# Kernel optimization log

Measured on AMD Instinct MI355X. Metric: run time of the kernel, lower is better.

Reference implementation:

```python
import jax, jax.numpy as jnp
import numpy as np

B, C, N = 4, 256, 4096
C4 = C // 4  # q/k projection dim (channels // 4)
BN_EPS = 1e-5


def setup_inputs() -> dict:
    key = jax.random.key(0)
    ks = jax.random.split(key, 4)
    s = 0.05
    return {
        "x": jax.random.normal(ks[0], (B, C, N), jnp.float32),
        # q_conv and k_conv share this weight in the original module
        "wq": jax.random.normal(ks[1], (C4, C), jnp.float32) * s,
        "wv": jax.random.normal(ks[2], (C, C), jnp.float32) * s,
        "bv": jnp.zeros((C,), jnp.float32),
        "wt": jax.random.normal(ks[3], (C, C), jnp.float32) * s,
        "bt": jnp.zeros((C,), jnp.float32),
        "gamma": jnp.ones((C,), jnp.float32),
        "beta": jnp.zeros((C,), jnp.float32),
        "running_mean": jnp.zeros((C,), jnp.float32),
        "running_var": jnp.ones((C,), jnp.float32),
    }


def reference(x, wq, wv, bv, wt, bt, gamma, beta, running_mean, running_var):
    # 1x1 Conv1d == channel matmul. q/k share wq.
    q = jnp.einsum('oc,bcn->bno', wq, x)            # [B, N, C4]
    k = jnp.einsum('oc,bcn->bon', wq, x)            # [B, C4, N]
    energy = jnp.einsum('bno,bom->bnm', q, k)       # [B, N, N]
    attn = jax.nn.softmax(energy, axis=-1)
    # offset-attention L1 re-normalization over dim 1 (query axis)
    attn = attn / (1e-9 + attn.sum(axis=1, keepdims=True))
    v = jnp.einsum('oc,bcn->bon', wv, x) + bv[None, :, None]   # [B, C, N]
    # x_r[b,c,n] = sum_m v[b,c,m] * attn[b,n,m]
    x_r = jnp.einsum('bcm,bnm->bcn', v, attn)       # [B, C, N]
    t = jnp.einsum('oc,bcn->bon', wt, x - x_r) + bt[None, :, None]
    # BatchNorm1d in inference mode (running stats)
    inv = jax.lax.rsqrt(running_var + BN_EPS)
    bn = (t - running_mean[None, :, None]) * (gamma * inv)[None, :, None] + beta[None, :, None]
    return x + jax.nn.relu(bn)
```

## Files before the change

### kernel.cpp

```cpp
#include <hip/hip_runtime.h>
#include <math.h>

namespace {

constexpr int B_ = 4;
constexpr int C_ = 256;
constexpr int C4_ = 64;
constexpr int N_ = 4096;

typedef __attribute__((ext_vector_type(8))) short bf16x8;
typedef __attribute__((ext_vector_type(4))) float f32x4;

__device__ __forceinline__ unsigned short bf16_rne(float f) {
    unsigned u = __float_as_uint(f);
    u += 0x7fffu + ((u >> 16) & 1u);
    return (unsigned short)(u >> 16);
}

__device__ __forceinline__ void g2l16(const unsigned short* g, unsigned short* l) {
    __builtin_amdgcn_global_load_lds(
        (const __attribute__((address_space(1))) unsigned int*)g,
        (__attribute__((address_space(3))) unsigned int*)l, 16, 0, 0);
}

__global__ __launch_bounds__(256) void cvt_kernel(
        const float* __restrict__ wq, const float* __restrict__ wv,
        const float* __restrict__ wt, unsigned short* __restrict__ wcomb,
        unsigned short* __restrict__ wtb) {
    const int i = (blockIdx.x * 256 + threadIdx.x) * 4;
    const float* src;
    unsigned short* dst;
    if (i < 16384) { src = wq + i; dst = wcomb + i; }
    else if (i < 81920) { src = wv + (i - 16384); dst = wcomb + i; }
    else { src = wt + (i - 81920); dst = wtb + (i - 81920); }
    const float4 f = *reinterpret_cast<const float4*>(src);
    ushort4 u;
    u.x = bf16_rne(f.x); u.y = bf16_rne(f.y);
    u.z = bf16_rne(f.z); u.w = bf16_rne(f.w);
    *reinterpret_cast<ushort4*>(dst) = u;
}

__global__ __launch_bounds__(1024, 4) void proj_kernel(
        const float* __restrict__ x, const unsigned short* __restrict__ wcomb,
        const float* __restrict__ bv, unsigned short* __restrict__ qkT,
        unsigned short* __restrict__ v) {
    __shared__ unsigned short xs[2][64][40];
    const int b = blockIdx.y;
    const int n0 = blockIdx.x * 64;
    const int tid = threadIdx.x;
    const int wave = tid >> 6, lane = tid & 63;
    const int ws = wave & 3, oq = wave >> 2;
    const int quad = lane >> 4, l15 = lane & 15;
    const int ca = tid >> 6, na = tid & 63;
    const int cb = (tid + 1024) >> 6, nb2 = (tid + 1024) & 63;
    f32x4 acc[5];
#pragma unroll
    for (int ot = 0; ot < 5; ++ot) acc[ot] = (f32x4){0.f, 0.f, 0.f, 0.f};
    xs[0][na][ca] = bf16_rne(x[((size_t)b * C_ + ca) * N_ + n0 + na]);
    xs[0][nb2][cb] = bf16_rne(x[((size_t)b * C_ + cb) * N_ + n0 + nb2]);
    __syncthreads();
    for (int ch = 0; ch < 8; ++ch) {
        const int buf = ch & 1;
        float la = 0.f, lb = 0.f;
        if (ch < 7) {
            la = x[((size_t)b * C_ + (ch + 1) * 32 + ca) * N_ + n0 + na];
            lb = x[((size_t)b * C_ + (ch + 1) * 32 + cb) * N_ + n0 + nb2];
        }
        const bf16x8 a = *reinterpret_cast<const bf16x8*>(&xs[buf][ws * 16 + l15][quad * 8]);
#pragma unroll
        for (int ot = 0; ot < 5; ++ot) {
            const int gro = oq * 5 + ot;
            const bf16x8 wb = *reinterpret_cast<const bf16x8*>(
                wcomb + (size_t)(gro * 16 + l15) * C_ + ch * 32 + quad * 8);
            acc[ot] = __builtin_amdgcn_mfma_f32_16x16x32_bf16(a, wb, acc[ot], 0, 0, 0);
        }
        if (ch < 7) {
            xs[buf ^ 1][na][ca] = bf16_rne(la);
            xs[buf ^ 1][nb2][cb] = bf16_rne(lb);
        }
        __syncthreads();
    }
    const int n = n0 + ws * 16 + quad * 4;
#pragma unroll
    for (int ot = 0; ot < 5; ++ot) {
        const int gro = oq * 5 + ot;
        if (gro < 4) {
            const int o = gro * 16 + l15;
#pragma unroll
            for (int r = 0; r < 4; ++r)
                qkT[((size_t)b * N_ + n + r) * C4_ + o] = bf16_rne(acc[ot][r]);
        } else {
            const int c = (gro - 4) * 16 + l15;
            const float bb = bv[c];
            ushort4 u;
            u.x = bf16_rne(acc[ot][0] + bb);
            u.y = bf16_rne(acc[ot][1] + bb);
            u.z = bf16_rne(acc[ot][2] + bb);
            u.w = bf16_rne(acc[ot][3] + bb);
            *reinterpret_cast<ushort4*>(&v[((size_t)b * C_ + c) * N_ + n]) = u;
        }
    }
}

__global__ __launch_bounds__(1024, 4) void rowsum_kernel(
        const unsigned short* __restrict__ qkT, float* __restrict__ rowsuminv) {
    __shared__ unsigned short kt[2][64][68];
    __shared__ float red[4][4][16];
    const int b = blockIdx.y;
    const int tid = threadIdx.x;
    const int wave = tid >> 6, lane = tid & 63;
    const int ws = wave & 3, sg = wave >> 2;
    const int quad = lane >> 4, l15 = lane & 15;
    const int n0 = blockIdx.x * 64;
    const unsigned short* qb = qkT + (size_t)b * N_ * C4_;
    const unsigned short* qrow = qb + (size_t)(n0 + ws * 16 + l15) * C4_;
    const bf16x8 a0 = *reinterpret_cast<const bf16x8*>(qrow + quad * 8);
    const bf16x8 a1 = *reinterpret_cast<const bf16x8*>(qrow + 32 + quad * 8);
    const int srow = tid >> 3, soff = tid & 7;
    if (tid < 512) {
        const bf16x8 sk = *reinterpret_cast<const bf16x8*>(qb + (size_t)srow * C4_ + soff * 8);
        *reinterpret_cast<bf16x8*>(&kt[0][srow][soff * 8]) = sk;
    }
    __syncthreads();
    float cs[4] = {};
    for (int mt = 0; mt < 64; ++mt) {
        const int buf = mt & 1;
        bf16x8 nk;
        if (mt < 63 && tid < 512)
            nk = *reinterpret_cast<const bf16x8*>(
                qb + (size_t)((mt + 1) * 64 + srow) * C4_ + soff * 8);
        const bf16x8 kb0 = *reinterpret_cast<const bf16x8*>(&kt[buf][sg * 16 + l15][quad * 8]);
        const bf16x8 kb1 = *reinterpret_cast<const bf16x8*>(&kt[buf][sg * 16 + l15][32 + quad * 8]);
        f32x4 z = {0.f, 0.f, 0.f, 0.f};
        z = __builtin_amdgcn_mfma_f32_16x16x32_bf16(a0, kb0, z, 0, 0, 0);
        const f32x4 e = __builtin_amdgcn_mfma_f32_16x16x32_bf16(a1, kb1, z, 0, 0, 0);
#pragma unroll
        for (int r = 0; r < 4; ++r) cs[r] += __expf(e[r]);
        if (mt < 63 && tid < 512)
            *reinterpret_cast<bf16x8*>(&kt[buf ^ 1][srow][soff * 8]) = nk;
        __syncthreads();
    }
#pragma unroll
    for (int r = 0; r < 4; ++r) {
#pragma unroll
        for (int k = 1; k <= 8; k <<= 1) cs[r] += __shfl_xor(cs[r], k, 64);
        if (l15 == 0) red[sg][ws][quad * 4 + r] = cs[r];
    }
    __syncthreads();
    if (tid < 64) {
        const int ws2 = tid >> 4, row = tid & 15;
        const float sum = red[0][ws2][row] + red[1][ws2][row] +
                          red[2][ws2][row] + red[3][ws2][row];
        rowsuminv[(size_t)b * N_ + n0 + ws2 * 16 + row] = 1.0f / sum;
    }
}

__global__ __launch_bounds__(1024, 4) void colsum_kernel(
        const unsigned short* __restrict__ qkT, const float* __restrict__ rowsuminv,
        float* __restrict__ colsuminv) {
    __shared__ float rl[N_];
    __shared__ unsigned short qt[2][64][68];
    __shared__ float red[4][4][16];
    const int b = blockIdx.y;
    const int tid = threadIdx.x;
    const int wave = tid >> 6, lane = tid & 63;
    const int mw = wave & 3, ng = wave >> 2;
    const int quad = lane >> 4, l15 = lane & 15;
    const int m0 = blockIdx.x * 64;
    for (int i = tid; i < N_; i += 1024) rl[i] = rowsuminv[(size_t)b * N_ + i];
    const unsigned short* qb = qkT + (size_t)b * N_ * C4_;
    const unsigned short* krow = qb + (size_t)(m0 + mw * 16 + l15) * C4_;
    const bf16x8 kb0 = *reinterpret_cast<const bf16x8*>(krow + quad * 8);
    const bf16x8 kb1 = *reinterpret_cast<const bf16x8*>(krow + 32 + quad * 8);
    const int srow = tid >> 3, soff = tid & 7;
    if (tid < 512) {
        const bf16x8 sq = *reinterpret_cast<const bf16x8*>(qb + (size_t)srow * C4_ + soff * 8);
        *reinterpret_cast<bf16x8*>(&qt[0][srow][soff * 8]) = sq;
    }
    __syncthreads();
    float cs = 0.f;
    for (int nt = 0; nt < 64; ++nt) {
        const int buf = nt & 1;
        bf16x8 nq;
        if (nt < 63 && tid < 512)
            nq = *reinterpret_cast<const bf16x8*>(
                qb + (size_t)((nt + 1) * 64 + srow) * C4_ + soff * 8);
        const bf16x8 a0 = *reinterpret_cast<const bf16x8*>(&qt[buf][ng * 16 + l15][quad * 8]);
        const bf16x8 a1 = *reinterpret_cast<const bf16x8*>(&qt[buf][ng * 16 + l15][32 + quad * 8]);
        f32x4 z = {0.f, 0.f, 0.f, 0.f};
        z = __builtin_amdgcn_mfma_f32_16x16x32_bf16(a0, kb0, z, 0, 0, 0);
        const f32x4 e = __builtin_amdgcn_mfma_f32_16x16x32_bf16(a1, kb1, z, 0, 0, 0);
        const int nb = nt * 64 + ng * 16 + quad * 4;
#pragma unroll
        for (int r = 0; r < 4; ++r) cs += __expf(e[r]) * rl[nb + r];
        if (nt < 63 && tid < 512)
            *reinterpret_cast<bf16x8*>(&qt[buf ^ 1][srow][soff * 8]) = nq;
        __syncthreads();
    }
    cs += __shfl_xor(cs, 16, 64);
    cs += __shfl_xor(cs, 32, 64);
    if (quad == 0) red[ng][mw][l15] = cs;
    __syncthreads();
    if (tid < 64) {
        const int mw2 = tid >> 4, l = tid & 15;
        const float sum = red[0][mw2][l] + red[1][mw2][l] +
                          red[2][mw2][l] + red[3][mw2][l];
        colsuminv[(size_t)b * N_ + m0 + mw2 * 16 + l] = 1.0f / (1e-9f + sum);
    }
}

__global__ __launch_bounds__(1024, 4) void final_kernel(
        const float* __restrict__ x, const unsigned short* __restrict__ qkT,
        const unsigned short* __restrict__ v, const unsigned short* __restrict__ wtb,
        const float* __restrict__ rowsuminv, const float* __restrict__ colsuminv,
        const float* __restrict__ bt, const float* __restrict__ gamma,
        const float* __restrict__ beta, const float* __restrict__ rmean,
        const float* __restrict__ rvar, float* __restrict__ out) {
    __shared__ union {
        struct {
            unsigned short vt[3][256][64];
            unsigned short kt[3][64][64];
        } s;
        unsigned short dsm[64][268];
    } u;
    __shared__ unsigned short p_sh[4][16][68];
    __shared__ float ci[N_];
    const int gid = blockIdx.x;
    const int xcd = gid & 7;
    const int b = xcd >> 1;
    const int n0 = ((((unsigned)gid >> 3) << 1) | (xcd & 1)) * 64;
    const int tid = threadIdx.x;
    const int wave = tid >> 6, lane = tid & 63;
    const int ws = wave & 3, g = wave >> 2;
    const int quad = lane >> 4, l15 = lane & 15;
    const unsigned short* qb = qkT + (size_t)b * N_ * C4_;
    const unsigned short* vbg = v + (size_t)b * C_ * N_;
    const int rowA = lane >> 3;
    const int swc = ((lane & 7) ^ rowA) * 8;
    const int w8 = wave * 8;
    const int r7 = l15 & 7;
    const int c0s = (quad * 8) ^ (r7 << 3);
    const int c1s = (32 + quad * 8) ^ (r7 << 3);
    const unsigned short* qrow = qb + (size_t)(n0 + ws * 16 + l15) * C4_;
    const bf16x8 q0 = *reinterpret_cast<const bf16x8*>(qrow + quad * 8);
    const bf16x8 q1 = *reinterpret_cast<const bf16x8*>(qrow + 32 + quad * 8);
    const float rli = rowsuminv[(size_t)b * N_ + n0 + ws * 16 + l15];
    {
        const float4 c4 = *reinterpret_cast<const float4*>(colsuminv + (size_t)b * N_ + tid * 4);
        *reinterpret_cast<float4*>(&ci[tid * 4]) = c4;
    }
#define STAGE_TILE(sidx, bufS)                                                          \
    do {                                                                                \
        g2l16(vbg + (size_t)(w8 + rowA) * N_ + (sidx) * 64 + swc,                       \
              &u.s.vt[bufS][w8][0]);                                                    \
        g2l16(vbg + (size_t)(w8 + 128 + rowA) * N_ + (sidx) * 64 + swc,                 \
              &u.s.vt[bufS][w8 + 128][0]);                                              \
        if (wave < 8)                                                                   \
            g2l16(qb + (size_t)((sidx) * 64 + w8 + rowA) * C4_ + swc,                   \
                  &u.s.kt[bufS][w8][0]);                                                \
    } while (0)
    STAGE_TILE(0, 0);
    STAGE_TILE(1, 1);
    if (wave < 8) asm volatile("s_waitcnt vmcnt(3)" ::: "memory");
    else          asm volatile("s_waitcnt vmcnt(2)" ::: "memory");
    asm volatile("s_waitcnt lgkmcnt(0)" ::: "memory");
    __builtin_amdgcn_s_barrier();
    f32x4 acc[4];
#pragma unroll
    for (int j = 0; j < 4; ++j) acc[j] = (f32x4){0.f, 0.f, 0.f, 0.f};
    int bufR = 0;
#pragma unroll 1
    for (int t = 0; t < 64; ++t) {
        if (t <= 61) {
            int bufS = bufR + 2; if (bufS >= 3) bufS -= 3;
            STAGE_TILE(t + 2, bufS);
        }
        {
            const unsigned short(*ktb)[64] = u.s.kt[bufR];
            const bf16x8 ka0 = *reinterpret_cast<const bf16x8*>(&ktb[g * 16 + l15][c0s]);
            const bf16x8 ka1 = *reinterpret_cast<const bf16x8*>(&ktb[g * 16 + l15][c1s]);
            f32x4 z = {0.f, 0.f, 0.f, 0.f};
            z = __builtin_amdgcn_mfma_f32_16x16x32_bf16(ka0, q0, z, 0, 0, 0);
            z = __builtin_amdgcn_mfma_f32_16x16x32_bf16(ka1, q1, z, 0, 0, 0);
            const float4 civ = *reinterpret_cast<const float4*>(&ci[t * 64 + g * 16 + quad * 4]);
            ushort4 pk;
            pk.x = bf16_rne(__expf(z[0]) * rli * civ.x);
            pk.y = bf16_rne(__expf(z[1]) * rli * civ.y);
            pk.z = bf16_rne(__expf(z[2]) * rli * civ.z);
            pk.w = bf16_rne(__expf(z[3]) * rli * civ.w);
            *reinterpret_cast<ushort4*>(&p_sh[ws][l15][g * 16 + quad * 4]) = pk;
        }
        asm volatile("s_waitcnt lgkmcnt(0)" ::: "memory");
        __builtin_amdgcn_s_barrier();
        {
            const bf16x8 pa0 = *reinterpret_cast<const bf16x8*>(&p_sh[ws][l15][quad * 8]);
            const bf16x8 pa1 = *reinterpret_cast<const bf16x8*>(&p_sh[ws][l15][32 + quad * 8]);
            const unsigned short(*vtb)[64] = u.s.vt[bufR];
#pragma unroll
            for (int j = 0; j < 4; ++j) {
                const int vr = (g * 4 + j) * 16 + l15;
                const bf16x8 vb0 = *reinterpret_cast<const bf16x8*>(&vtb[vr][c0s]);
                const bf16x8 vb1 = *reinterpret_cast<const bf16x8*>(&vtb[vr][c1s]);
                acc[j] = __builtin_amdgcn_mfma_f32_16x16x32_bf16(pa0, vb0, acc[j], 0, 0, 0);
                acc[j] = __builtin_amdgcn_mfma_f32_16x16x32_bf16(pa1, vb1, acc[j], 0, 0, 0);
            }
        }
        asm volatile("s_waitcnt lgkmcnt(0)" ::: "memory");
        if (t <= 61) {
            if (wave < 8) asm volatile("s_waitcnt vmcnt(3)" ::: "memory");
            else          asm volatile("s_waitcnt vmcnt(2)" ::: "memory");
        } else {
            asm volatile("s_waitcnt vmcnt(0)" ::: "memory");
        }
        __builtin_amdgcn_s_barrier();
        ++bufR; if (bufR >= 3) bufR = 0;
    }
#undef STAGE_TILE
#pragma unroll
    for (int j = 0; j < 4; ++j) {
        const int c = (g * 4 + j) * 16 + l15;
        const float4 xv = *reinterpret_cast<const float4*>(
            &x[((size_t)b * C_ + c) * N_ + n0 + ws * 16 + quad * 4]);
        const float xvr[4] = {xv.x, xv.y, xv.z, xv.w};
#pragma unroll
        for (int r = 0; r < 4; ++r)
            u.dsm[ws * 16 + quad * 4 + r][c] = bf16_rne(xvr[r] - acc[j][r]);
    }
    __syncthreads();
    bf16x8 da[8];
#pragma unroll
    for (int k = 0; k < 8; ++k)
        da[k] = *reinterpret_cast<const bf16x8*>(&u.dsm[ws * 16 + l15][k * 32 + quad * 8]);
    f32x4 tacc[4];
#pragma unroll
    for (int j = 0; j < 4; ++j) tacc[j] = (f32x4){0.f, 0.f, 0.f, 0.f};
#pragma unroll
    for (int j = 0; j < 4; ++j) {
        const int ot = g * 4 + j;
#pragma unroll
        for (int k = 0; k < 8; ++k) {
            const bf16x8 wb = *reinterpret_cast<const bf16x8*>(
                wtb + (size_t)(ot * 16 + l15) * C_ + k * 32 + quad * 8);
            tacc[j] = __builtin_amdgcn_mfma_f32_16x16x32_bf16(da[k], wb, tacc[j], 0, 0, 0);
        }
    }
#pragma unroll
    for (int j = 0; j < 4; ++j) {
        const int o = (g * 4 + j) * 16 + l15;
        const float gg = gamma[o] * rsqrtf(rvar[o] + 1e-5f);
        const float mn = rmean[o], bbet = beta[o], bo = bt[o];
        const size_t oi = ((size_t)b * C_ + o) * N_ + n0 + ws * 16 + quad * 4;
        const float4 xo = *reinterpret_cast<const float4*>(&x[oi]);
        float4 res;
        res.x = xo.x + fmaxf((tacc[j][0] + bo - mn) * gg + bbet, 0.f);
        res.y = xo.y + fmaxf((tacc[j][1] + bo - mn) * gg + bbet, 0.f);
        res.z = xo.z + fmaxf((tacc[j][2] + bo - mn) * gg + bbet, 0.f);
        res.w = xo.w + fmaxf((tacc[j][3] + bo - mn) * gg + bbet, 0.f);
        *reinterpret_cast<float4*>(&out[oi]) = res;
    }
}

}

extern "C" void kernel_launch(void* const* d_in, const int* in_sizes, int n_in,
                              void* d_out, int out_size, void* d_ws, size_t ws_size,
                              hipStream_t stream) {
    const float* x = (const float*)d_in[0];
    const float* wq = (const float*)d_in[1];
    const float* wv = (const float*)d_in[2];
    const float* bv = (const float*)d_in[3];
    const float* wt = (const float*)d_in[4];
    const float* bt = (const float*)d_in[5];
    const float* gamma = (const float*)d_in[6];
    const float* beta = (const float*)d_in[7];
    const float* rmean = (const float*)d_in[8];
    const float* rvar = (const float*)d_in[9];
    float* out = (float*)d_out;

    char* base = (char*)d_ws;
    unsigned short* qkT = (unsigned short*)base;
    unsigned short* vw = (unsigned short*)(base + (2u << 20));
    unsigned short* wtb = (unsigned short*)(base + (10u << 20));
    unsigned short* wcomb = (unsigned short*)(base + (10u << 20) + (128u << 10));
    float* rowsuminv = (float*)(base + (10u << 20) + (288u << 10));
    float* colsuminv = (float*)(base + (10u << 20) + (352u << 10));

    cvt_kernel<<<dim3(144), dim3(256), 0, stream>>>(wq, wv, wt, wcomb, wtb);
    proj_kernel<<<dim3(N_ / 64, B_), dim3(1024), 0, stream>>>(x, wcomb, bv, qkT, vw);
    rowsum_kernel<<<dim3(N_ / 64, B_), dim3(1024), 0, stream>>>(qkT, rowsuminv);
    colsum_kernel<<<dim3(N_ / 64, B_), dim3(1024), 0, stream>>>(qkT, rowsuminv, colsuminv);
    final_kernel<<<dim3(N_ / 64 * B_), dim3(1024), 0, stream>>>(
        x, qkT, vw, wtb, rowsuminv, colsuminv, bt, gamma, beta, rmean, rvar, out);
}
```

Baseline: 267.9 us.

## Triple-buffer rowsum/colsum with async LDS loads, XCD-aware block mapping, MFMA priority

The rowsum and colsum kernels now stage K/Q tiles into a 3-deep swizzled LDS ring using direct global-to-LDS loads, replacing the register round-trip double buffer and __syncthreads. Fine-grained vmcnt waits and raw barriers take the place of the old synchronisation. Blocks are remapped over a flat grid so each XCD handles one batch, which should improve L2 locality. s_setprio is raised around MFMA sections in all three attention kernels to favour matrix issue, at the cost of more complex wait-count bookkeeping that must stay correct.

```diff
diff --git a/kernel.cpp b/kernel.cpp
--- a/kernel.cpp
+++ b/kernel.cpp
@@ -104,42 +104,60 @@
 
 __global__ __launch_bounds__(1024, 4) void rowsum_kernel(
         const unsigned short* __restrict__ qkT, float* __restrict__ rowsuminv) {
-    __shared__ unsigned short kt[2][64][68];
+    __shared__ unsigned short kt[3][64][64];
     __shared__ float red[4][4][16];
-    const int b = blockIdx.y;
+    const int gid = blockIdx.x;
+    const int xcd = gid & 7;
+    const int b = xcd >> 1;
+    const int n0 = ((((unsigned)gid >> 3) << 1) | (xcd & 1)) * 64;
     const int tid = threadIdx.x;
     const int wave = tid >> 6, lane = tid & 63;
     const int ws = wave & 3, sg = wave >> 2;
     const int quad = lane >> 4, l15 = lane & 15;
-    const int n0 = blockIdx.x * 64;
     const unsigned short* qb = qkT + (size_t)b * N_ * C4_;
+    const int rowA = lane >> 3;
+    const int swc = ((lane & 7) ^ rowA) * 8;
+    const int w8 = wave * 8;
+    const int r7 = l15 & 7;
+    const int c0s = (quad * 8) ^ (r7 << 3);
+    const int c1s = (32 + quad * 8) ^ (r7 << 3);
     const unsigned short* qrow = qb + (size_t)(n0 + ws * 16 + l15) * C4_;
     const bf16x8 a0 = *reinterpret_cast<const bf16x8*>(qrow + quad * 8);
     const bf16x8 a1 = *reinterpret_cast<const bf16x8*>(qrow + 32 + quad * 8);
-    const int srow = tid >> 3, soff = tid & 7;
-    if (tid < 512) {
-        const bf16x8 sk = *reinterpret_cast<const bf16x8*>(qb + (size_t)srow * C4_ + soff * 8);
-        *reinterpret_cast<bf16x8*>(&kt[0][srow][soff * 8]) = sk;
-    }
-    __syncthreads();
+    asm volatile("s_waitcnt vmcnt(0)" ::: "memory");
+#define RS_STAGE(sidx, bufS)                                                  \
+    if (wave < 8) g2l16(qb + (size_t)((sidx) * 64 + w8 + rowA) * C4_ + swc,   \
+                        &kt[bufS][w8][0]);
+    RS_STAGE(0, 0);
+    RS_STAGE(1, 1);
+    if (wave < 8) asm volatile("s_waitcnt vmcnt(1)" ::: "memory");
+    __builtin_amdgcn_s_barrier();
     float cs[4] = {};
+    int bufR = 0;
+#pragma unroll 1
     for (int mt = 0; mt < 64; ++mt) {
-        const int buf = mt & 1;
-        bf16x8 nk;
-        if (mt < 63 && tid < 512)
-            nk = *reinterpret_cast<const bf16x8*>(
-                qb + (size_t)((mt + 1) * 64 + srow) * C4_ + soff * 8);
-        const bf16x8 kb0 = *reinterpret_cast<const bf16x8*>(&kt[buf][sg * 16 + l15][quad * 8]);
-        const bf16x8 kb1 = *reinterpret_cast<const bf16x8*>(&kt[buf][sg * 16 + l15][32 + quad * 8]);
+        if (mt <= 61) {
+            int bufS = bufR + 2; if (bufS >= 3) bufS -= 3;
+            RS_STAGE(mt + 2, bufS);
+        }
+        const bf16x8 kb0 = *reinterpret_cast<const bf16x8*>(&kt[bufR][sg * 16 + l15][c0s]);
+        const bf16x8 kb1 = *reinterpret_cast<const bf16x8*>(&kt[bufR][sg * 16 + l15][c1s]);
+        __builtin_amdgcn_s_setprio(1);
         f32x4 z = {0.f, 0.f, 0.f, 0.f};
         z = __builtin_amdgcn_mfma_f32_16x16x32_bf16(a0, kb0, z, 0, 0, 0);
         const f32x4 e = __builtin_amdgcn_mfma_f32_16x16x32_bf16(a1, kb1, z, 0, 0, 0);
-#pragma unroll
-        for (int r = 0; r < 4; ++r) cs[r] += __expf(e[r]);
-        if (mt < 63 && tid < 512)
-            *reinterpret_cast<bf16x8*>(&kt[buf ^ 1][srow][soff * 8]) = nk;
-        __syncthreads();
-    }
+        __builtin_amdgcn_s_setprio(0);
+        cs[0] += __expf(e[0]); cs[1] += __expf(e[1]);
+        cs[2] += __expf(e[2]); cs[3] += __expf(e[3]);
+        asm volatile("s_waitcnt lgkmcnt(0)" ::: "memory");
+        if (wave < 8) {
+            if (mt <= 61)      asm volatile("s_waitcnt vmcnt(1)" ::: "memory");
+            else if (mt == 62) asm volatile("s_waitcnt vmcnt(0)" ::: "memory");
+        }
+        __builtin_amdgcn_s_barrier();
+        ++bufR; if (bufR >= 3) bufR = 0;
+    }
+#undef RS_STAGE
 #pragma unroll
     for (int r = 0; r < 4; ++r) {
 #pragma unroll
@@ -159,44 +177,63 @@
         const unsigned short* __restrict__ qkT, const float* __restrict__ rowsuminv,
         float* __restrict__ colsuminv) {
     __shared__ float rl[N_];
-    __shared__ unsigned short qt[2][64][68];
+    __shared__ unsigned short qt[3][64][64];
     __shared__ float red[4][4][16];
-    const int b = blockIdx.y;
+    const int gid = blockIdx.x;
+    const int xcd = gid & 7;
+    const int b = xcd >> 1;
+    const int m0 = ((((unsigned)gid >> 3) << 1) | (xcd & 1)) * 64;
     const int tid = threadIdx.x;
     const int wave = tid >> 6, lane = tid & 63;
     const int mw = wave & 3, ng = wave >> 2;
     const int quad = lane >> 4, l15 = lane & 15;
-    const int m0 = blockIdx.x * 64;
+    const unsigned short* qb = qkT + (size_t)b * N_ * C4_;
+    const int rowA = lane >> 3;
+    const int swc = ((lane & 7) ^ rowA) * 8;
+    const int w8 = wave * 8;
+    const int r7 = l15 & 7;
+    const int c0s = (quad * 8) ^ (r7 << 3);
+    const int c1s = (32 + quad * 8) ^ (r7 << 3);
     for (int i = tid; i < N_; i += 1024) rl[i] = rowsuminv[(size_t)b * N_ + i];
-    const unsigned short* qb = qkT + (size_t)b * N_ * C4_;
     const unsigned short* krow = qb + (size_t)(m0 + mw * 16 + l15) * C4_;
     const bf16x8 kb0 = *reinterpret_cast<const bf16x8*>(krow + quad * 8);
     const bf16x8 kb1 = *reinterpret_cast<const bf16x8*>(krow + 32 + quad * 8);
-    const int srow = tid >> 3, soff = tid & 7;
-    if (tid < 512) {
-        const bf16x8 sq = *reinterpret_cast<const bf16x8*>(qb + (size_t)srow * C4_ + soff * 8);
-        *reinterpret_cast<bf16x8*>(&qt[0][srow][soff * 8]) = sq;
-    }
-    __syncthreads();
+    asm volatile("s_waitcnt vmcnt(0)" ::: "memory");
+#define CS_STAGE(sidx, bufS)                                                  \
+    if (wave < 8) g2l16(qb + (size_t)((sidx) * 64 + w8 + rowA) * C4_ + swc,   \
+                        &qt[bufS][w8][0]);
+    CS_STAGE(0, 0);
+    CS_STAGE(1, 1);
+    if (wave < 8) asm volatile("s_waitcnt vmcnt(1)" ::: "memory");
+    asm volatile("s_waitcnt lgkmcnt(0)" ::: "memory");
+    __builtin_amdgcn_s_barrier();
     float cs = 0.f;
+    int bufR = 0;
+#pragma unroll 1
     for (int nt = 0; nt < 64; ++nt) {
-        const int buf = nt & 1;
-        bf16x8 nq;
-        if (nt < 63 && tid < 512)
-            nq = *reinterpret_cast<const bf16x8*>(
-                qb + (size_t)((nt + 1) * 64 + srow) * C4_ + soff * 8);
-        const bf16x8 a0 = *reinterpret_cast<const bf16x8*>(&qt[buf][ng * 16 + l15][quad * 8]);
-        const bf16x8 a1 = *reinterpret_cast<const bf16x8*>(&qt[buf][ng * 16 + l15][32 + quad * 8]);
+        if (nt <= 61) {
+            int bufS = bufR + 2; if (bufS >= 3) bufS -= 3;
+            CS_STAGE(nt + 2, bufS);
+        }
+        const bf16x8 a0 = *reinterpret_cast<const bf16x8*>(&qt[bufR][ng * 16 + l15][c0s]);
+        const bf16x8 a1 = *reinterpret_cast<const bf16x8*>(&qt[bufR][ng * 16 + l15][c1s]);
+        __builtin_amdgcn_s_setprio(1);
         f32x4 z = {0.f, 0.f, 0.f, 0.f};
         z = __builtin_amdgcn_mfma_f32_16x16x32_bf16(a0, kb0, z, 0, 0, 0);
         const f32x4 e = __builtin_amdgcn_mfma_f32_16x16x32_bf16(a1, kb1, z, 0, 0, 0);
+        __builtin_amdgcn_s_setprio(0);
         const int nb = nt * 64 + ng * 16 + quad * 4;
 #pragma unroll
         for (int r = 0; r < 4; ++r) cs += __expf(e[r]) * rl[nb + r];
-        if (nt < 63 && tid < 512)
-            *reinterpret_cast<bf16x8*>(&qt[buf ^ 1][srow][soff * 8]) = nq;
-        __syncthreads();
-    }
+        asm volatile("s_waitcnt lgkmcnt(0)" ::: "memory");
+        if (wave < 8) {
+            if (nt <= 61)      asm volatile("s_waitcnt vmcnt(1)" ::: "memory");
+            else if (nt == 62) asm volatile("s_waitcnt vmcnt(0)" ::: "memory");
+        }
+        __builtin_amdgcn_s_barrier();
+        ++bufR; if (bufR >= 3) bufR = 0;
+    }
+#undef CS_STAGE
     cs += __shfl_xor(cs, 16, 64);
     cs += __shfl_xor(cs, 32, 64);
     if (quad == 0) red[ng][mw][l15] = cs;
@@ -249,6 +286,7 @@
         const float4 c4 = *reinterpret_cast<const float4*>(colsuminv + (size_t)b * N_ + tid * 4);
         *reinterpret_cast<float4*>(&ci[tid * 4]) = c4;
     }
+    asm volatile("s_waitcnt vmcnt(0)" ::: "memory");
 #define STAGE_TILE(sidx, bufS)                                                          \
     do {                                                                                \
         g2l16(vbg + (size_t)(w8 + rowA) * N_ + (sidx) * 64 + swc,                       \
@@ -279,9 +317,11 @@
             const unsigned short(*ktb)[64] = u.s.kt[bufR];
             const bf16x8 ka0 = *reinterpret_cast<const bf16x8*>(&ktb[g * 16 + l15][c0s]);
             const bf16x8 ka1 = *reinterpret_cast<const bf16x8*>(&ktb[g * 16 + l15][c1s]);
+            __builtin_amdgcn_s_setprio(1);
             f32x4 z = {0.f, 0.f, 0.f, 0.f};
             z = __builtin_amdgcn_mfma_f32_16x16x32_bf16(ka0, q0, z, 0, 0, 0);
             z = __builtin_amdgcn_mfma_f32_16x16x32_bf16(ka1, q1, z, 0, 0, 0);
+            __builtin_amdgcn_s_setprio(0);
             const float4 civ = *reinterpret_cast<const float4*>(&ci[t * 64 + g * 16 + quad * 4]);
             ushort4 pk;
             pk.x = bf16_rne(__expf(z[0]) * rli * civ.x);
@@ -296,6 +336,7 @@
             const bf16x8 pa0 = *reinterpret_cast<const bf16x8*>(&p_sh[ws][l15][quad * 8]);
             const bf16x8 pa1 = *reinterpret_cast<const bf16x8*>(&p_sh[ws][l15][32 + quad * 8]);
             const unsigned short(*vtb)[64] = u.s.vt[bufR];
+            __builtin_amdgcn_s_setprio(1);
 #pragma unroll
             for (int j = 0; j < 4; ++j) {
                 const int vr = (g * 4 + j) * 16 + l15;
@@ -304,6 +345,7 @@
                 acc[j] = __builtin_amdgcn_mfma_f32_16x16x32_bf16(pa0, vb0, acc[j], 0, 0, 0);
                 acc[j] = __builtin_amdgcn_mfma_f32_16x16x32_bf16(pa1, vb1, acc[j], 0, 0, 0);
             }
+            __builtin_amdgcn_s_setprio(0);
         }
         asm volatile("s_waitcnt lgkmcnt(0)" ::: "memory");
         if (t <= 61) {
@@ -387,8 +429,8 @@
 
     cvt_kernel<<<dim3(144), dim3(256), 0, stream>>>(wq, wv, wt, wcomb, wtb);
     proj_kernel<<<dim3(N_ / 64, B_), dim3(1024), 0, stream>>>(x, wcomb, bv, qkT, vw);
-    rowsum_kernel<<<dim3(N_ / 64, B_), dim3(1024), 0, stream>>>(qkT, rowsuminv);
-    colsum_kernel<<<dim3(N_ / 64, B_), dim3(1024), 0, stream>>>(qkT, rowsuminv, colsuminv);
+    rowsum_kernel<<<dim3(N_ / 64 * B_), dim3(1024), 0, stream>>>(qkT, rowsuminv);
+    colsum_kernel<<<dim3(N_ / 64 * B_), dim3(1024), 0, stream>>>(qkT, rowsuminv, colsuminv);
     final_kernel<<<dim3(N_ / 64 * B_), dim3(1024), 0, stream>>>(
         x, qkT, vw, wtb, rowsuminv, colsuminv, bt, gamma, beta, rmean, rvar, out);
 }
```

After: 260.0 us. -2.9%, faster.
